# Optimization experiments

Measured on AMD Instinct MI355X. Metric: run time of the kernel, lower is better.

## Reference

```python
import math
import jax, jax.numpy as jnp
import numpy as np

B, CIN, COUT, H, W, K, SDIM = 8, 32, 32, 512, 512, 3, 512


def setup_inputs() -> dict:
    key = jax.random.key(0)
    k1, k2, k3, k4 = jax.random.split(key, 4)
    return {
        "x": jax.random.normal(k1, (B, CIN, H, W), dtype=jnp.float32),
        "style": jax.random.normal(k2, (B, SDIM), dtype=jnp.float32),
        "weight": jax.random.normal(k3, (1, COUT, CIN, K, K), dtype=jnp.float32),
        "mod_w": jax.random.normal(k4, (CIN, SDIM), dtype=jnp.float32),
        "mod_b": jnp.zeros((CIN,), dtype=jnp.float32),
    }


def reference(x, style, weight, mod_w, mod_b):
    # x: [B, Cin, H, W]; style: [B, S]; weight: [1, Cout, Cin, K, K]
    b, cin, h, w = x.shape
    _, cout, _, k, _ = weight.shape
    sdim = mod_w.shape[1]

    # EqualLinear modulation: out = style @ (W * scale)^T + bias * lr_mul (lr_mul=1)
    mod_scale = 1.0 / math.sqrt(sdim)
    s = style @ (mod_w * mod_scale).T + mod_b  # [B, Cin]

    # Per-sample weight modulation + demodulation
    conv_scale = 1.0 / math.sqrt(cin * k * k)
    wmod = conv_scale * weight * s[:, None, :, None, None]  # [B, Cout, Cin, K, K]
    demod = jax.lax.rsqrt(jnp.sum(wmod * wmod, axis=(2, 3, 4)) + 1e-8)  # [B, Cout]
    wmod = wmod * demod[:, :, None, None, None]

    pad = k // 2

    def conv_one(xi, wi):
        # xi: [Cin, H, W], wi: [Cout, Cin, K, K]
        return jax.lax.conv_general_dilated(
            xi[None], wi, window_strides=(1, 1),
            padding=[(pad, pad), (pad, pad)],
            dimension_numbers=("NCHW", "OIHW", "NCHW"),
        )[0]

    out = jax.vmap(conv_one)(x, wmod)  # [B, Cout, H, W]
    return out
```

## Files before the change

kernel.cpp:

```cpp
#include <hip/hip_runtime.h>

#define B_    8
#define CIN   32
#define COUT  32
#define H_    512
#define W_    512
#define SDIM  512

#define MOD_SCALE  0.044194173824159216f
#define CONV_SCALE 0.05892556509887896f

#define PXB 64
#define RB  4
#define LR  6
#define LW  66

typedef unsigned short u16;
typedef __attribute__((ext_vector_type(8))) short           bf16x8;
typedef __attribute__((ext_vector_type(4))) float           f32x4;

__device__ __forceinline__ u16 f2bf(float x) {
    union { float f; unsigned u; } v; v.f = x;
    unsigned r = v.u + 0x7FFFu + ((v.u >> 16) & 1u);
    return (u16)(r >> 16);
}
__device__ __forceinline__ float bf2f(u16 h) {
    union { float f; unsigned u; } v; v.u = ((unsigned)h) << 16;
    return v.f;
}

__global__ __launch_bounds__(64) void modweights_kernel(
    const float* __restrict__ style,
    const float* __restrict__ weight,
    const float* __restrict__ mod_w,
    const float* __restrict__ mod_b,
    u16* __restrict__ wh,
    u16* __restrict__ wl)
{
    const int b  = blockIdx.x / COUT;
    const int co = blockIdx.x % COUT;
    const int t  = threadIdx.x;

    __shared__ float s_sh[CIN];

    const float4* st4 = (const float4*)(style + (size_t)b * SDIM);
    const float4 sv0 = st4[t];
    const float4 sv1 = st4[t + 64];

    for (int ci = 0; ci < CIN; ++ci) {
        const float4* mw4 = (const float4*)(mod_w + (size_t)ci * SDIM);
        const float4 a = mw4[t];
        const float4 c = mw4[t + 64];
        float p = sv0.x*a.x + sv0.y*a.y + sv0.z*a.z + sv0.w*a.w
                + sv1.x*c.x + sv1.y*c.y + sv1.z*c.z + sv1.w*c.w;
        #pragma unroll
        for (int off = 32; off > 0; off >>= 1) p += __shfl_xor(p, off);
        if (t == 0) s_sh[ci] = p * MOD_SCALE + mod_b[ci];
    }
    __syncthreads();

    const float* wco = weight + (size_t)co * CIN * 9;

    float ss = 0.f;
    for (int i = t; i < CIN * 9; i += 64) {
        const float v = CONV_SCALE * wco[i] * s_sh[i / 9];
        ss += v * v;
    }
    #pragma unroll
    for (int off = 32; off > 0; off >>= 1) ss += __shfl_xor(ss, off);
    const float dem = rsqrtf(ss + 1e-8f);

    for (int i = t; i < CIN * 9; i += 64) {
        const int ci  = i / 9;
        const int ofs = i - ci * 9;
        const float v = CONV_SCALE * wco[i] * s_sh[ci] * dem;
        const size_t o = (((size_t)b * 9 + ofs) * COUT + co) * CIN + ci;
        const u16 hb = f2bf(v);
        wh[o] = hb;
        wl[o] = f2bf(v - bf2f(hb));
    }
}

__global__ __launch_bounds__(256) void conv_kernel(
    const float* __restrict__ x,
    const u16* __restrict__ wh,
    const u16* __restrict__ wl,
    float* __restrict__ out)
{
    __shared__ u16 xh[LR * LW * CIN];
    __shared__ u16 xl[LR * LW * CIN];

    const int t  = threadIdx.x;
    const int w0 = blockIdx.x * PXB;
    const int h0 = blockIdx.y * RB;
    const int b  = blockIdx.z;

    const int lane = t & 63;
    const int wid  = t >> 6;
    const int wm   = wid >> 1;
    const int wn   = wid & 1;
    const int l15  = lane & 15;
    const int k0   = (lane >> 4) * 8;

    bf16x8 ah[9], al[9];
    #pragma unroll
    for (int ofs = 0; ofs < 9; ++ofs) {
        const size_t o = (((size_t)b * 9 + ofs) * COUT + wm * 16 + l15) * CIN + k0;
        ah[ofs] = *(const bf16x8*)(wh + o);
        al[ofs] = *(const bf16x8*)(wl + o);
    }

    for (int task = t; task < LR * 4 * LW; task += 256) {
        const int w  = task % LW;
        const int rc = task / LW;
        const int r  = rc >> 2;
        const int cg = rc & 3;
        const int gw = w0 + w - 1;
        const int ih = h0 + r - 1;
        float v[8];
        if ((unsigned)ih < (unsigned)H_ && (unsigned)gw < (unsigned)W_) {
            const float* p = x + ((size_t)(b * CIN + cg * 8) * H_ + ih) * W_ + gw;
            #pragma unroll
            for (int j = 0; j < 8; ++j) v[j] = p[(size_t)j * H_ * W_];
        } else {
            #pragma unroll
            for (int j = 0; j < 8; ++j) v[j] = 0.f;
        }
        unsigned hu[4], lu[4];
        #pragma unroll
        for (int q = 0; q < 4; ++q) {
            const u16 h0b = f2bf(v[2*q]);
            const u16 h1b = f2bf(v[2*q+1]);
            const u16 l0b = f2bf(v[2*q]   - bf2f(h0b));
            const u16 l1b = f2bf(v[2*q+1] - bf2f(h1b));
            hu[q] = (unsigned)h0b | ((unsigned)h1b << 16);
            lu[q] = (unsigned)l0b | ((unsigned)l1b << 16);
        }
        const int idx = (((r * LW + w) * CIN) + cg * 8) ^ ((w & 7) << 3);
        *(uint4*)(xh + idx) = make_uint4(hu[0], hu[1], hu[2], hu[3]);
        *(uint4*)(xl + idx) = make_uint4(lu[0], lu[1], lu[2], lu[3]);
    }
    __syncthreads();

    f32x4 acc[RB][2];
    #pragma unroll
    for (int r = 0; r < RB; ++r) {
        acc[r][0] = (f32x4){0.f, 0.f, 0.f, 0.f};
        acc[r][1] = (f32x4){0.f, 0.f, 0.f, 0.f};
    }

    #pragma unroll
    for (int r_in = 0; r_in < LR; ++r_in) {
        #pragma unroll
        for (int sub = 0; sub < 2; ++sub) {
            bf16x8 bh[3], bl[3];
            #pragma unroll
            for (int kw = 0; kw < 3; ++kw) {
                const int wl_ = wn * 32 + sub * 16 + l15 + kw;
                const int idx = (((r_in * LW + wl_) * CIN) + k0) ^ ((wl_ & 7) << 3);
                bh[kw] = *(const bf16x8*)(xh + idx);
                bl[kw] = *(const bf16x8*)(xl + idx);
            }
            #pragma unroll
            for (int kh = 0; kh < 3; ++kh) {
                const int r_out = r_in - kh;
                if (r_out < 0 || r_out >= RB) continue;
                #pragma unroll
                for (int kw = 0; kw < 3; ++kw) {
                    const int tap = kh * 3 + kw;
                    acc[r_out][sub] = __builtin_amdgcn_mfma_f32_16x16x32_bf16(
                        ah[tap], bh[kw], acc[r_out][sub], 0, 0, 0);
                    acc[r_out][sub] = __builtin_amdgcn_mfma_f32_16x16x32_bf16(
                        ah[tap], bl[kw], acc[r_out][sub], 0, 0, 0);
                    acc[r_out][sub] = __builtin_amdgcn_mfma_f32_16x16x32_bf16(
                        al[tap], bh[kw], acc[r_out][sub], 0, 0, 0);
                }
            }
        }
    }

    #pragma unroll
    for (int r = 0; r < RB; ++r) {
        #pragma unroll
        for (int sub = 0; sub < 2; ++sub) {
            const int opx = w0 + wn * 32 + sub * 16 + l15;
            #pragma unroll
            for (int j = 0; j < 4; ++j) {
                const int oco = wm * 16 + (lane >> 4) * 4 + j;
                out[(((size_t)b * COUT + oco) * H_ + h0 + r) * W_ + opx] = acc[r][sub][j];
            }
        }
    }
}

extern "C" void kernel_launch(void* const* d_in, const int* in_sizes, int n_in,
                              void* d_out, int out_size, void* d_ws, size_t ws_size,
                              hipStream_t stream)
{
    const float* x      = (const float*)d_in[0];
    const float* style  = (const float*)d_in[1];
    const float* weight = (const float*)d_in[2];
    const float* mod_w  = (const float*)d_in[3];
    const float* mod_b  = (const float*)d_in[4];
    float* out = (float*)d_out;

    u16* wh = (u16*)d_ws;
    u16* wl = wh + (size_t)B_ * 9 * COUT * CIN;

    modweights_kernel<<<B_ * COUT, 64, 0, stream>>>(style, weight, mod_w, mod_b, wh, wl);

    dim3 grid(W_ / PXB, H_ / RB, B_);
    conv_kernel<<<grid, 256, 0, stream>>>(x, wh, wl, out);
}
```

Baseline: 531.1 us.

## Replace split-bf16 triple MFMA with single fp16 MFMA and swizzle block order

Drops the hi/lo bf16 split emulation (three MFMAs per tap and two LDS tiles) in favour of a single fp16 conversion of inputs and modulated weights with one fp16 MFMA per tap. This cuts matrix-core work, LDS footprint and conversion ALU work. Block indices are also remapped so consecutive workgroups spread across batch/row tiles, aiming at better cache or XCD locality. The cost is lower numerical accuracy, with about 11-bit mantissa products, which may exceed tolerance.

```diff
diff --git a/kernel.cpp b/kernel.cpp
--- a/kernel.cpp
+++ b/kernel.cpp
@@ -16,26 +16,15 @@
 #define LW  66
 
 typedef unsigned short u16;
-typedef __attribute__((ext_vector_type(8))) short           bf16x8;
+typedef __attribute__((ext_vector_type(8))) _Float16        f16x8;
 typedef __attribute__((ext_vector_type(4))) float           f32x4;
-
-__device__ __forceinline__ u16 f2bf(float x) {
-    union { float f; unsigned u; } v; v.f = x;
-    unsigned r = v.u + 0x7FFFu + ((v.u >> 16) & 1u);
-    return (u16)(r >> 16);
-}
-__device__ __forceinline__ float bf2f(u16 h) {
-    union { float f; unsigned u; } v; v.u = ((unsigned)h) << 16;
-    return v.f;
-}
 
 __global__ __launch_bounds__(64) void modweights_kernel(
     const float* __restrict__ style,
     const float* __restrict__ weight,
     const float* __restrict__ mod_w,
     const float* __restrict__ mod_b,
-    u16* __restrict__ wh,
-    u16* __restrict__ wl)
+    u16* __restrict__ w16)
 {
     const int b  = blockIdx.x / COUT;
     const int co = blockIdx.x % COUT;
@@ -75,25 +64,26 @@
         const int ofs = i - ci * 9;
         const float v = CONV_SCALE * wco[i] * s_sh[ci] * dem;
         const size_t o = (((size_t)b * 9 + ofs) * COUT + co) * CIN + ci;
-        const u16 hb = f2bf(v);
-        wh[o] = hb;
-        wl[o] = f2bf(v - bf2f(hb));
+        w16[o] = __builtin_bit_cast(u16, (_Float16)v);
     }
 }
 
 __global__ __launch_bounds__(256) void conv_kernel(
     const float* __restrict__ x,
-    const u16* __restrict__ wh,
-    const u16* __restrict__ wl,
+    const u16* __restrict__ w16,
     float* __restrict__ out)
 {
-    __shared__ u16 xh[LR * LW * CIN];
-    __shared__ u16 xl[LR * LW * CIN];
+    __shared__ u16 xs[LR * LW * CIN];
+
+    const int flat = blockIdx.x + (blockIdx.y << 3) + (blockIdx.z << 10);
+    const int swz  = ((flat & 7) << 10) | (flat >> 3);
+    const int bx   = swz & 7;
+    const int by   = (swz >> 3) & 127;
+    const int b    = swz >> 10;
 
     const int t  = threadIdx.x;
-    const int w0 = blockIdx.x * PXB;
-    const int h0 = blockIdx.y * RB;
-    const int b  = blockIdx.z;
+    const int w0 = bx * PXB;
+    const int h0 = by * RB;
 
     const int lane = t & 63;
     const int wid  = t >> 6;
@@ -102,12 +92,11 @@
     const int l15  = lane & 15;
     const int k0   = (lane >> 4) * 8;
 
-    bf16x8 ah[9], al[9];
+    f16x8 af[9];
     #pragma unroll
     for (int ofs = 0; ofs < 9; ++ofs) {
         const size_t o = (((size_t)b * 9 + ofs) * COUT + wm * 16 + l15) * CIN + k0;
-        ah[ofs] = *(const bf16x8*)(wh + o);
-        al[ofs] = *(const bf16x8*)(wl + o);
+        af[ofs] = *(const f16x8*)(w16 + o);
     }
 
     for (int task = t; task < LR * 4 * LW; task += 256) {
@@ -126,19 +115,15 @@
             #pragma unroll
             for (int j = 0; j < 8; ++j) v[j] = 0.f;
         }
-        unsigned hu[4], lu[4];
+        unsigned hu[4];
         #pragma unroll
         for (int q = 0; q < 4; ++q) {
-            const u16 h0b = f2bf(v[2*q]);
-            const u16 h1b = f2bf(v[2*q+1]);
-            const u16 l0b = f2bf(v[2*q]   - bf2f(h0b));
-            const u16 l1b = f2bf(v[2*q+1] - bf2f(h1b));
-            hu[q] = (unsigned)h0b | ((unsigned)h1b << 16);
-            lu[q] = (unsigned)l0b | ((unsigned)l1b << 16);
+            const u16 a = __builtin_bit_cast(u16, (_Float16)v[2*q]);
+            const u16 c = __builtin_bit_cast(u16, (_Float16)v[2*q+1]);
+            hu[q] = (unsigned)a | ((unsigned)c << 16);
         }
         const int idx = (((r * LW + w) * CIN) + cg * 8) ^ ((w & 7) << 3);
-        *(uint4*)(xh + idx) = make_uint4(hu[0], hu[1], hu[2], hu[3]);
-        *(uint4*)(xl + idx) = make_uint4(lu[0], lu[1], lu[2], lu[3]);
+        *(uint4*)(xs + idx) = make_uint4(hu[0], hu[1], hu[2], hu[3]);
     }
     __syncthreads();
 
@@ -153,13 +138,12 @@
     for (int r_in = 0; r_in < LR; ++r_in) {
         #pragma unroll
         for (int sub = 0; sub < 2; ++sub) {
-            bf16x8 bh[3], bl[3];
+            f16x8 bf[3];
             #pragma unroll
             for (int kw = 0; kw < 3; ++kw) {
                 const int wl_ = wn * 32 + sub * 16 + l15 + kw;
                 const int idx = (((r_in * LW + wl_) * CIN) + k0) ^ ((wl_ & 7) << 3);
-                bh[kw] = *(const bf16x8*)(xh + idx);
-                bl[kw] = *(const bf16x8*)(xl + idx);
+                bf[kw] = *(const f16x8*)(xs + idx);
             }
             #pragma unroll
             for (int kh = 0; kh < 3; ++kh) {
@@ -167,13 +151,8 @@
                 if (r_out < 0 || r_out >= RB) continue;
                 #pragma unroll
                 for (int kw = 0; kw < 3; ++kw) {
-                    const int tap = kh * 3 + kw;
-                    acc[r_out][sub] = __builtin_amdgcn_mfma_f32_16x16x32_bf16(
-                        ah[tap], bh[kw], acc[r_out][sub], 0, 0, 0);
-                    acc[r_out][sub] = __builtin_amdgcn_mfma_f32_16x16x32_bf16(
-                        ah[tap], bl[kw], acc[r_out][sub], 0, 0, 0);
-                    acc[r_out][sub] = __builtin_amdgcn_mfma_f32_16x16x32_bf16(
-                        al[tap], bh[kw], acc[r_out][sub], 0, 0, 0);
+                    acc[r_out][sub] = __builtin_amdgcn_mfma_f32_16x16x32_f16(
+                        af[kh * 3 + kw], bf[kw], acc[r_out][sub], 0, 0, 0);
                 }
             }
         }
@@ -204,11 +183,10 @@
     const float* mod_b  = (const float*)d_in[4];
     float* out = (float*)d_out;
 
-    u16* wh = (u16*)d_ws;
-    u16* wl = wh + (size_t)B_ * 9 * COUT * CIN;
+    u16* w16 = (u16*)d_ws;
 
-    modweights_kernel<<<B_ * COUT, 64, 0, stream>>>(style, weight, mod_w, mod_b, wh, wl);
+    modweights_kernel<<<B_ * COUT, 64, 0, stream>>>(style, weight, mod_w, mod_b, w16);
 
     dim3 grid(W_ / PXB, H_ / RB, B_);
-    conv_kernel<<<grid, 256, 0, stream>>>(x, wh, wl, out);
+    conv_kernel<<<grid, 256, 0, stream>>>(x, w16, out);
 }
```

Result: faster. 494.6 us (-6.9%).
